# Kernel tuning notes

Measured on AMD Instinct MI355X. Metric: run time of the kernel, lower is better.

The kernel has to match this reference:

```python
import jax, jax.numpy as jnp
import numpy as np

EPS = 1e-5  # BatchNorm eps (eval mode, running_mean=0, running_var=1)

def bn(z, gamma, beta):
    s = gamma / jnp.sqrt(1.0 + EPS)
    return z * s[None, :, None, None] + beta[None, :, None, None]

def conv1d(x, w, b, pad):
    # x: (N,C,L), w: (O,C,K)
    y = jax.lax.conv_general_dilated(x, w, (1,), [(pad, pad)],
                                     dimension_numbers=('NCH', 'OIH', 'NCH'))
    return y + b[None, :, None]

def setup_inputs():
    key = jax.random.key(0)
    N, C, T, V = 128, 64, 128, 25
    S, H = 3, 8
    ig = C // 4   # gcn q/k embedding channels
    ih = C // H   # per-head channels
    ks = iter(jax.random.split(key, 40))
    rn = lambda shape, s=0.05: jax.random.normal(next(ks), shape, jnp.float32) * s
    inp = {}
    inp['x'] = jax.random.normal(next(ks), (N, C, T, V), jnp.float32)
    inp['A'] = jnp.stack([jnp.eye(V, dtype=jnp.float32)] * S) + jax.random.uniform(next(ks), (S, V, V), jnp.float32) * 0.05
    inp['alpha'] = jnp.float32(0.1)
    inp['Wq'] = rn((S, ig, C)); inp['bq'] = rn((S, ig))
    inp['Wk'] = rn((S, ig, C)); inp['bk'] = rn((S, ig))
    inp['Wf'] = rn((S, C, C)); inp['bf'] = rn((S, C))
    inp['g_gamma'] = jnp.ones((C,), jnp.float32); inp['g_beta'] = jnp.zeros((C,), jnp.float32)
    inp['W_sa'] = rn((1, C, V)); inp['b_sa'] = rn((1,))
    inp['W_ta'] = rn((1, C, 9)); inp['b_ta'] = rn((1,))
    inp['W_fc1'] = rn((C // 2, C)); inp['b_fc1'] = rn((C // 2,))
    inp['W_fc2'] = rn((C, C // 2)); inp['b_fc2'] = rn((C,))
    inp['pos_emb'] = rn((1, T, C * V), 0.02)
    inp['Wq_h'] = rn((H, ih, C)); inp['bq_h'] = rn((H, ih))
    inp['Wk_h'] = rn((H, ih, C)); inp['bk_h'] = rn((H, ih))
    inp['Wv_h'] = rn((H, ih, C)); inp['bv_h'] = rn((H, ih))
    inp['W_ffn'] = rn((C, C)); inp['b_ffn'] = rn((C,))
    inp['m_gamma'] = jnp.ones((C,), jnp.float32); inp['m_beta'] = jnp.zeros((C,), jnp.float32)
    return inp

def reference(x, A, alpha, Wq, bq, Wk, bk, Wf, bf, g_gamma, g_beta,
              W_sa, b_sa, W_ta, b_ta, W_fc1, b_fc1, W_fc2, b_fc2,
              pos_emb, Wq_h, bq_h, Wk_h, bk_h, Wv_h, bv_h,
              W_ffn, b_ffn, m_gamma, m_beta):
    N, C, T, V = x.shape
    S, ig = Wq.shape[0], Wq.shape[1]
    # ---------- unit_gcn_qkv (adaptive graph conv) ----------
    q = jnp.einsum('sic,nctv->nsitv', Wq, x) + bq[None, :, :, None, None]
    k = jnp.einsum('sic,nctv->nsitv', Wk, x) + bk[None, :, :, None, None]
    qf = q.transpose(0, 1, 4, 2, 3).reshape(N, S, V, ig * T)   # (N,S,V,ig*T)
    kf = k.reshape(N, S, ig * T, V)                            # (N,S,ig*T,V)
    att = jnp.einsum('nsvd,nsdw->nsvw', qf, kf) / jnp.float32(ig * T)
    att = jax.nn.softmax(att, axis=-2)                         # Softmax(dim=-2)
    Aad = A[None] + att * alpha                                # (N,S,V,V)
    xf = x.reshape(N, C * T, V)
    agg = jnp.einsum('ndv,nsvw->nsdw', xf, Aad).reshape(N, S, C, T, V)
    y = jnp.einsum('soc,nsctv->notv', Wf, agg) + bf.sum(0)[None, :, None, None]
    y = bn(y, g_gamma, g_beta) + x                             # down = identity (in==out)
    y = jax.nn.relu(y)
    # spatial / temporal / channel attention gates (MS-AAGCN style)
    se = y.mean(axis=2)                                        # (N,C,V)
    sa = jax.nn.sigmoid(conv1d(se, W_sa, b_sa, (V - 1) // 2))  # (N,1,V)
    y = y * sa[:, :, None, :] + y
    se = y.mean(axis=3)                                        # (N,C,T)
    ta = jax.nn.sigmoid(conv1d(se, W_ta, b_ta, 4))             # (N,1,T)
    y = y * ta[:, :, :, None] + y
    se = y.mean(axis=(2, 3))                                   # (N,C)
    ca = jax.nn.sigmoid(jax.nn.relu(se @ W_fc1.T + b_fc1) @ W_fc2.T + b_fc2)
    y = y * ca[:, :, None, None] + y
    # ---------- Multi-Head causal Temporal Attention ----------
    pe = pos_emb.reshape(1, T, C, V).transpose(0, 2, 1, 3)     # 'n t (d v)' -> 'n d t v'
    xa = y + pe
    H, ih = Wq_h.shape[0], Wq_h.shape[1]
    d = ih * V
    qh = (jnp.einsum('hoc,nctv->nhtov', Wq_h, xa) + bq_h[None, :, None, :, None]).reshape(N, H, T, d)
    kh = (jnp.einsum('hoc,nctv->nhtov', Wk_h, xa) + bk_h[None, :, None, :, None]).reshape(N, H, T, d)
    vh = (jnp.einsum('hoc,nctv->nhtov', Wv_h, xa) + bv_h[None, :, None, :, None]).reshape(N, H, T, d)
    scores = jnp.einsum('nhtd,nhsd->nhts', qh, kh) / jnp.sqrt(jnp.float32(d))
    causal = jnp.tril(jnp.ones((T, T), bool))
    scores = jnp.where(causal[None, None], scores, jnp.float32(-1e9))
    p = jax.nn.softmax(scores, axis=-1)
    oh = jnp.einsum('nhts,nhsd->nhtd', p, vh)
    # concat heads along emb dim, reinterpret '(d v)' -> channels-major layout
    z = oh.reshape(N, H, T, ih, V).transpose(0, 1, 3, 2, 4).reshape(N, C, T, V)
    z = bn(z, m_gamma, m_beta) + xa
    z = jax.nn.relu(jnp.einsum('oc,nctv->notv', W_ffn, z) + b_ffn[None, :, None, None]) + xa
    z = bn(z, m_gamma, m_beta)
    # ---------- unit residual ----------
    return jax.nn.relu(z + x)
```

## Files before the change

### kernel.cpp

```cpp
#include <hip/hip_runtime.h>
#include <hip/hip_bf16.h>

#define N_ 128
#define C_ 64
#define T_ 128
#define V_ 25
#define S_ 3
#define IG 16
#define IH 8
#define H_ 8
#define D_ 200
#define CV 1600
#define TV 3200
#define EPSB 1e-5f
#define NCHUNK 16

typedef __attribute__((ext_vector_type(8))) short short8v;
typedef __attribute__((ext_vector_type(4))) float f32x4;
#define MFMA16 __builtin_amdgcn_mfma_f32_16x16x32_bf16
#define ZIDX(r,c) ((r)*72 + ((c) ^ ((((r)>>3)&7)<<3)))

__device__ __forceinline__ float sigm(float x){ return 1.f/(1.f+expf(-x)); }
__device__ __forceinline__ float b2f(__hip_bfloat16 b){ return __bfloat162float(b); }
__device__ __forceinline__ __hip_bfloat16 f2b(float f){ return __float2bfloat16(f); }
__device__ __forceinline__ float ubl(unsigned int u){ return __uint_as_float(u<<16); }
__device__ __forceinline__ float ubh(unsigned int u){ return __uint_as_float(u & 0xffff0000u); }
__device__ __forceinline__ float sh2f(short s){ return __uint_as_float(((unsigned int)(unsigned short)s)<<16); }
__device__ __forceinline__ unsigned short f2bu(float f){
  unsigned int u = __float_as_uint(f);
  u += 0x7fff + ((u>>16)&1);
  return (unsigned short)(u>>16);
}
__device__ __forceinline__ unsigned long long pk4bf(f32x4 v){
  unsigned long long a = f2bu(v[0]);
  unsigned long long b = f2bu(v[1]);
  unsigned long long c = f2bu(v[2]);
  unsigned long long d = f2bu(v[3]);
  return a | (b<<16) | (c<<32) | (d<<48);
}

__global__ __launch_bounds__(256) void k_prep(
    const float* __restrict__ Wq, const float* __restrict__ Wk,
    const float* __restrict__ Wf,
    const float* __restrict__ Wq_h, const float* __restrict__ Wk_h,
    const float* __restrict__ Wv_h, const float* __restrict__ W_ffn,
    short* __restrict__ wqb, short* __restrict__ wkb, short* __restrict__ Wfb,
    short* __restrict__ w3b, short* __restrict__ Wffnb)
{
  const int i = blockIdx.x*256 + threadIdx.x;
  if (i < 3072){ wqb[i]=(short)f2bu(Wq[i]); wkb[i]=(short)f2bu(Wk[i]); }
  if (i < 12288) Wfb[i]=(short)f2bu(Wf[i]);
  if (i < 4096){
    w3b[i]      =(short)f2bu(Wq_h[i]);
    w3b[4096+i] =(short)f2bu(Wk_h[i]);
    w3b[8192+i] =(short)f2bu(Wv_h[i]);
    Wffnb[i]    =(short)f2bu(W_ffn[i]);
  }
}

__global__ __launch_bounds__(256) void k_gcn_att1(
    const float* __restrict__ x,
    const short* __restrict__ wqb, const float* __restrict__ bq,
    const short* __restrict__ wkb, const float* __restrict__ bk,
    float* __restrict__ attg)
{
  const int tc = blockIdx.x, n = blockIdx.y;
  const int tid = threadIdx.x;
  const int wv = tid>>6, l = tid&63, lc = l&15, lk = l>>4;
  __shared__ __align__(16) short xtb[4*32*72];
  __shared__ __align__(16) char QB[3*32*256];
  __shared__ __align__(16) char KB[3*32*256];
  __shared__ float bql[48], bkl[48];
  short8v aqf[3][2], akf[3][2];
  #pragma unroll
  for (int s=0;s<3;++s){
    #pragma unroll
    for (int ks=0;ks<2;++ks){
      aqf[s][ks] = *(const short8v*)(wqb + (s*16+lc)*64 + ks*32 + lk*8);
      akf[s][ks] = *(const short8v*)(wkb + (s*16+lc)*64 + ks*32 + lk*8);
    }
  }
  if (tid<48){ bql[tid]=bq[tid]; bkl[tid]=bk[tid]; }
  for (int i=tid;i<4*7*72;i+=256){
    int tl=i/(7*72), r=i%(7*72);
    xtb[(tl*32+25)*72 + r] = 0;
  }
  const float* xn = x + (size_t)n*C_*TV;
  #pragma unroll
  for (int tg=0; tg<2; ++tg){
    if (tg) __syncthreads();
    {
      const int base = tc*200 + tg*100;
      float4 xb[7];
      #pragma unroll
      for (int k=0;k<7;++k){
        int i = tid + k*256;
        if (i<1600){ int c=i/25,a=i%25; xb[k] = *(const float4*)(xn + (size_t)c*TV + base + a*4); }
      }
      #pragma unroll
      for (int k=0;k<7;++k){
        int i = tid + k*256;
        if (i<1600){
          int c=i/25,a=i%25;
          float xv[4]={xb[k].x,xb[k].y,xb[k].z,xb[k].w};
          #pragma unroll
          for (int j=0;j<4;++j){
            int tv=a*4+j, tl=tv/25, v=tv-tl*25;
            xtb[(tl*32+v)*72 + c] = (short)f2bu(xv[j]);
          }
        }
      }
    }
    __syncthreads();
    const int tcol = (tg*4+wv)*32;
    const int sw = (lc&7)<<4;
    #pragma unroll
    for (int s=0;s<3;++s){
      f32x4 z={0.f,0.f,0.f,0.f};
      f32x4 aq0=z,aq1=z,ak0=z,ak1=z;
      #pragma unroll
      for (int ks=0;ks<2;++ks){
        short8v b0 = *(const short8v*)(xtb + (wv*32+lc)*72 + ks*32 + lk*8);
        short8v b1 = *(const short8v*)(xtb + (wv*32+16+lc)*72 + ks*32 + lk*8);
        aq0 = MFMA16(aqf[s][ks], b0, aq0,0,0,0);
        aq1 = MFMA16(aqf[s][ks], b1, aq1,0,0,0);
        ak0 = MFMA16(akf[s][ks], b0, ak0,0,0,0);
        ak1 = MFMA16(akf[s][ks], b1, ak1,0,0,0);
      }
      f32x4 q0,q1,k0,k1;
      #pragma unroll
      for (int r=0;r<4;++r){
        float bqv=bql[s*16+lk*4+r], bkv=bkl[s*16+lk*4+r];
        q0[r]=aq0[r]+bqv; q1[r]=aq1[r]+bqv;
        k0[r]=ak0[r]+bkv; k1[r]=ak1[r]+bkv;
      }
      char* QBs = QB + s*8192;
      char* KBs = KB + s*8192;
      *(unsigned long long*)(QBs + ((lc*256      + tcol + lk*8) ^ sw)) = pk4bf(q0);
      *(unsigned long long*)(QBs + (((16+lc)*256 + tcol + lk*8) ^ sw)) = pk4bf(q1);
      *(unsigned long long*)(KBs + ((lc*256      + tcol + lk*8) ^ sw)) = pk4bf(k0);
      *(unsigned long long*)(KBs + (((16+lc)*256 + tcol + lk*8) ^ sw)) = pk4bf(k1);
    }
  }
  __syncthreads();
  const int mt = wv>>1, nt = wv&1;
  const int sw = (lc&7)<<4;
  #pragma unroll
  for (int s=0;s<3;++s){
    const char* QBs = QB + s*8192;
    const char* KBs = KB + s*8192;
    f32x4 acc = {0.f,0.f,0.f,0.f};
    #pragma unroll
    for (int ks=0;ks<4;++ks){
      short8v a = *(const short8v*)(QBs + (((mt*16+lc)*256 + ks*64 + lk*16) ^ sw));
      short8v b = *(const short8v*)(KBs + (((nt*16+lc)*256 + ks*64 + lk*16) ^ sw));
      acc = MFMA16(a,b,acc,0,0,0);
    }
    float* Ao = attg + ((size_t)tc*(N_*S_) + n*S_ + s)*(V_*V_);
    #pragma unroll
    for (int reg=0;reg<4;++reg){
      int v = mt*16 + lk*4 + reg, w = nt*16 + lc;
      if (v<V_ && w<V_) Ao[v*V_+w] = acc[reg];
    }
  }
}

__global__ __launch_bounds__(256) void k_gcn_att2(
    const float* __restrict__ attg, const float* __restrict__ A,
    const float* __restrict__ alphap, short* __restrict__ AsTg)
{
  const int ns = blockIdx.x, s = ns % S_, tid = threadIdx.x;
  __shared__ float att[V_*V_];
  short* dst = AsTg + (size_t)ns*1280;
  for (int i=tid;i<1280;i+=256) dst[i]=0;
  for (int i=tid;i<V_*V_;i+=256){
    float acc=0.f;
    #pragma unroll
    for (int tcc=0;tcc<NCHUNK;++tcc) acc += attg[((size_t)tcc*(N_*S_) + ns)*(V_*V_) + i];
    att[i]=acc;
  }
  __syncthreads();
  if (tid<V_){
    const int w=tid; const float inv=1.f/(IG*T_);
    float mx=-1e30f;
    for (int v=0;v<V_;++v) mx=fmaxf(mx, att[v*V_+w]*inv);
    float sum=0.f;
    for (int v=0;v<V_;++v){ float e=expf(att[v*V_+w]*inv-mx); att[v*V_+w]=e; sum+=e; }
    float rs=1.f/sum;
    for (int v=0;v<V_;++v) att[v*V_+w]*=rs;
  }
  __syncthreads();
  const float alpha=alphap[0];
  for (int i=tid;i<V_*V_;i+=256){
    int v=i/25, w=i%25;
    dst[w*40+v] = (short)f2bu(A[s*625+i] + alpha*att[i]);
  }
}

__global__ __launch_bounds__(256) void k_gcn_y(
    const float* __restrict__ x, const short* __restrict__ AsTg,
    const short* __restrict__ Wfb, const float* __restrict__ bfp,
    const float* __restrict__ g_gamma, const float* __restrict__ g_beta,
    __hip_bfloat16* __restrict__ y1)
{
  const int tc=blockIdx.x, n=blockIdx.y, tid=threadIdx.x;
  const int wv=tid>>6, l=tid&63, lc=l&15, lk=l>>4;
  __shared__ __align__(16) short xtb[64*136];
  __shared__ __align__(16) short AsT[3*32*40];
  __shared__ __align__(16) short aggT[112*200];
  const float* xn = x + (size_t)n*C_*TV;
  const int tv0 = tc*100;
  float4 xbuf[7];
  #pragma unroll
  for (int k=0;k<7;++k){
    int i = tid + k*256;
    if (i < 1600){
      int c=i/25, a=i%25;
      xbuf[k] = *(const float4*)(xn + (size_t)c*TV + tv0 + a*4);
    }
  }
  #pragma unroll
  for (int k=0;k<7;++k){
    int i = tid + k*256;
    if (i < 1600){
      int c=i/25, a=i%25, tv4=a*4;
      float xv[4] = {xbuf[k].x, xbuf[k].y, xbuf[k].z, xbuf[k].w};
      #pragma unroll
      for (int j=0;j<4;++j){
        int tv=tv4+j, t=tv/25, v=tv-t*25;
        xtb[c*136 + t*32 + v] = (short)f2bu(xv[j]);
      }
    }
  }
  for (int i=tid;i<64*28;i+=256){ int c=i/28, r=i%28; xtb[c*136 + (r/7)*32 + 25 + (r%7)] = 0; }
  {
    const short* As_g = AsTg + (size_t)n*3840;
    for (int i=tid;i<480;i+=256)
      *(short8v*)(AsT + i*8) = *(const short8v*)(As_g + i*8);
  }
  for (int i=tid;i<12*200;i+=256) aggT[100*200+i]=0;
  __syncthreads();
  {
    const int t = wv;
    for (int s=0;s<S_;++s){
      short8v b0 = *(const short8v*)(AsT + (s*32+lc)*40 + lk*8);
      short8v b1 = *(const short8v*)(AsT + (s*32+16+lc)*40 + lk*8);
      #pragma unroll
      for (int mt=0;mt<4;++mt){
        short8v a = *(const short8v*)(xtb + (mt*16+lc)*136 + t*32 + lk*8);
        f32x4 z={0.f,0.f,0.f,0.f};
        f32x4 acc0 = MFMA16(a,b0,z,0,0,0);
        f32x4 acc1 = MFMA16(a,b1,z,0,0,0);
        *(unsigned long long*)(aggT + (t*25+lc)*200 + s*64 + mt*16 + lk*4) = pk4bf(acc0);
        if (lc<9)
          *(unsigned long long*)(aggT + (t*25+16+lc)*200 + s*64 + mt*16 + lk*4) = pk4bf(acc1);
      }
    }
  }
  short8v af[6];
  #pragma unroll
  for (int ks=0;ks<6;++ks){
    const int s = ks>>1, c0 = (ks&1)*32 + lk*8;
    af[ks] = *(const short8v*)(Wfb + (size_t)(s*C_ + wv*16+lc)*C_ + c0);
  }
  __syncthreads();
  f32x4 acc[7];
  #pragma unroll
  for (int dt=0;dt<7;++dt) acc[dt]=(f32x4){0.f,0.f,0.f,0.f};
  #pragma unroll
  for (int dt=0;dt<7;++dt){
    #pragma unroll
    for (int ks=0;ks<6;++ks){
      short8v b = *(const short8v*)(aggT + (dt*16+lc)*200 + ks*32 + lk*8);
      acc[dt] = MFMA16(af[ks], b, acc[dt],0,0,0);
    }
  }
  const float invs = rsqrtf(1.f+EPSB);
  __hip_bfloat16* yo = y1 + (size_t)n*C_*TV;
  #pragma unroll
  for (int reg=0;reg<4;++reg){
    const int o = wv*16 + lk*4 + reg;
    const float bsum = bfp[o]+bfp[C_+o]+bfp[2*C_+o];
    const float gs = g_gamma[o]*invs, gb = g_beta[o];
    #pragma unroll
    for (int dt=0;dt<7;++dt){
      const int tv = dt*16 + lc;
      if (tv < 100){
        const int t = tv/25, v = tv - t*25;
        float xres = sh2f(xtb[o*136 + t*32 + v]);
        float val = (acc[dt][reg]+bsum)*gs + gb + xres;
        yo[(size_t)o*TV + tv0 + tv] = f2b(fmaxf(val,0.f));
      }
    }
  }
}

__global__ __launch_bounds__(256) void k_seT(const __hip_bfloat16* __restrict__ y1,
    float* __restrict__ seT)
{
  const int c=blockIdx.x, n=blockIdx.y, tid=threadIdx.x;
  const int v = tid&31, g = tid>>5;
  __shared__ float red[8][33];
  const __hip_bfloat16* yp = y1 + ((size_t)n*C_+c)*T_*V_;
  float s=0.f;
  if (v < V_){
    #pragma unroll 4
    for (int j=0;j<16;++j){
      int t = g + j*8;
      s += b2f(yp[t*V_+v]);
    }
  }
  red[g][v]=s;
  __syncthreads();
  if (tid < V_){
    float tot=0.f;
    #pragma unroll
    for (int g2=0;g2<8;++g2) tot += red[g2][tid];
    seT[((size_t)n*C_+c)*V_+tid]=tot*(1.f/T_);
  }
}

__global__ __launch_bounds__(256) void k_sa(const float* __restrict__ seT,
    const float* __restrict__ W_sa, const float* __restrict__ b_sa,
    float* __restrict__ sa)
{
  const int n=blockIdx.x, tid=threadIdx.x;
  __shared__ float sel[CV];
  __shared__ float wsl[CV];
  __shared__ float part[8][32];
  const float* se = seT + (size_t)n*C_*V_;
  for (int i=tid;i<CV;i+=256){ sel[i]=se[i]; wsl[i]=W_sa[i]; }
  __syncthreads();
  if (tid < 200){
    const int v = tid%25, cg = tid/25;
    float acc=0.f;
    for (int c=cg*8;c<cg*8+8;++c){
      #pragma unroll
      for (int k=0;k<V_;++k){
        int vv=v+k-12;
        if (vv>=0&&vv<V_) acc += sel[c*V_+vv]*wsl[c*V_+k];
      }
    }
    part[cg][v]=acc;
  }
  __syncthreads();
  if (tid<V_){
    float acc=b_sa[0];
    #pragma unroll
    for (int g=0;g<8;++g) acc+=part[g][tid];
    sa[n*V_+tid]=sigm(acc);
  }
}

__global__ __launch_bounds__(256) void k_seV(const __hip_bfloat16* __restrict__ y1,
    const float* __restrict__ sa, float* __restrict__ seV)
{
  const int c=blockIdx.x, n=blockIdx.y, tid=threadIdx.x;
  const int v = tid&31, g = tid>>5;
  __shared__ float sal[32];
  if (tid<32) sal[tid] = (tid<V_)? 1.f+sa[n*V_+tid] : 0.f;
  __syncthreads();
  const __hip_bfloat16* yp = y1 + ((size_t)n*C_+c)*T_*V_;
  float* svo = seV + ((size_t)n*C_+c)*T_;
  const float sv_ = sal[v];
  for (int j=0;j<16;++j){
    int t = g*16 + j;
    float val = (v<V_)? b2f(yp[t*V_+v])*sv_ : 0.f;
    #pragma unroll
    for (int off=16;off;off>>=1) val += __shfl_xor(val, off);
    if (v==0) svo[t]=val*(1.f/V_);
  }
}

__global__ __launch_bounds__(256) void k_ta_ca(const float* __restrict__ seV,
    const float* __restrict__ W_ta, const float* __restrict__ b_ta,
    const float* __restrict__ W_fc1, const float* __restrict__ b_fc1,
    const float* __restrict__ W_fc2, const float* __restrict__ b_fc2,
    float* __restrict__ ta, float* __restrict__ ca)
{
  const int n=blockIdx.x, tid=threadIdx.x;
  __shared__ float svl[C_*T_];
  __shared__ float wtl[C_*9];
  __shared__ float w1l[32*C_];
  __shared__ float w2l[C_*32];
  __shared__ float tal[T_];
  __shared__ float part2[2][T_];
  __shared__ float part4[C_][4];
  __shared__ float scls[C_];
  __shared__ float h1[32];
  const float* sv = seV + (size_t)n*C_*T_;
  for (int i=tid;i<C_*T_;i+=256) svl[i]=sv[i];
  for (int i=tid;i<C_*9;i+=256) wtl[i]=W_ta[i];
  for (int i=tid;i<32*C_;i+=256){ w1l[i]=W_fc1[i]; w2l[i]=W_fc2[i]; }
  __syncthreads();
  {
    const int t = tid & 127, half = tid >> 7;
    float acc = 0.f;
    for (int c=half*32; c<half*32+32; ++c){
      #pragma unroll
      for (int k=0;k<9;++k){
        int tt=t+k-4;
        if (tt>=0&&tt<T_) acc += svl[c*T_+tt]*wtl[c*9+k];
      }
    }
    part2[half][t]=acc;
  }
  __syncthreads();
  if (tid<T_){
    float s_=sigm(part2[0][tid]+part2[1][tid]+b_ta[0]);
    tal[tid]=s_; ta[n*T_+tid]=s_;
  }
  __syncthreads();
  {
    const int c = tid>>2, q = tid&3;
    float acc=0.f;
    for (int t=q*32;t<q*32+32;++t) acc += svl[c*T_+t]*(1.f+tal[t]);
    part4[c][q]=acc;
  }
  __syncthreads();
  if (tid<C_) scls[tid]=(part4[tid][0]+part4[tid][1]+part4[tid][2]+part4[tid][3])*(1.f/T_);
  __syncthreads();
  if (tid<32){
    float acc=b_fc1[tid];
    for (int c=0;c<C_;++c) acc += scls[c]*w1l[tid*C_+c];
    h1[tid]=fmaxf(acc,0.f);
  }
  __syncthreads();
  if (tid<C_){
    float acc=b_fc2[tid];
    for (int j=0;j<32;++j) acc += h1[j]*w2l[tid*32+j];
    ca[n*C_+tid]=sigm(acc);
  }
}

__global__ __launch_bounds__(256) void k_xa_qkv(
    const __hip_bfloat16* __restrict__ y1, const float* __restrict__ pos_emb,
    const float* __restrict__ sa, const float* __restrict__ ta, const float* __restrict__ ca,
    const short* __restrict__ w3b, const float* __restrict__ bq_h,
    const float* __restrict__ bk_h, const float* __restrict__ bv_h,
    __hip_bfloat16* __restrict__ xa, __hip_bfloat16* __restrict__ qb,
    __hip_bfloat16* __restrict__ kb, __hip_bfloat16* __restrict__ vb)
{
  const int tc=blockIdx.x, n=blockIdx.y, tid=threadIdx.x;
  const int wv=tid>>6, l=tid&63, lc=l&15, lk=l>>4;
  __shared__ __align__(16) short w3[192*72];
  __shared__ __align__(16) short xalT[4][32*72];
  __shared__ float bl[192];
  __shared__ float sal[32], cal[64], tgs[4];
  const int tv0 = tc*100;
  const __hip_bfloat16* y1n = y1 + (size_t)n*C_*TV;
  __hip_bfloat16* xan = xa + (size_t)n*C_*TV;
  uint2 ybuf[7];
  #pragma unroll
  for (int k=0;k<7;++k){
    int i = tid + k*256;
    if (i < 1600){
      int c=i/25, a=i%25;
      ybuf[k] = *(const uint2*)(y1n + (size_t)c*TV + tv0 + a*4);
    }
  }
  for (int i=tid;i<1536;i+=256){
    int mu=i>>3, j=i&7;
    *(short8v*)(w3 + mu*72 + j*8) = *(const short8v*)(w3b + mu*64 + j*8);
  }
  if (tid<192){
    int which=tid/C_, ho=tid%C_;
    bl[tid] = (which==0?bq_h:(which==1?bk_h:bv_h))[ho];
  }
  if (tid<32) sal[tid] = (tid<V_)? 1.f+sa[n*V_+tid] : 0.f;
  if (tid>=32 && tid<96) cal[tid-32] = 1.f+ca[n*C_+tid-32];
  if (tid>=96 && tid<100) tgs[tid-96] = 1.f+ta[n*T_+tc*4+(tid-96)];
  for (int i=tid;i<4*7*72;i+=256){
    int tl=i/(7*72), r=i%(7*72);
    xalT[tl][25*72 + r] = 0;
  }
  __syncthreads();
  #pragma unroll
  for (int k=0;k<7;++k){
    int i = tid + k*256;
    if (i < 1600){
      int c=i/25, a=i%25, tv4=a*4;
      unsigned int u0=ybuf[k].x, u1=ybuf[k].y;
      float yv[4] = {ubl(u0),ubh(u0),ubl(u1),ubh(u1)};
      const float calc = cal[c];
      unsigned long long pack = 0ull;
      #pragma unroll
      for (int j=0;j<4;++j){
        int tv=tv4+j, tl=tv/25, v=tv-tl*25;
        float val = yv[j]*sal[v]*tgs[tl]*calc + pos_emb[(size_t)(tc*4+tl)*CV + c*V_ + v];
        unsigned short b = f2bu(val);
        pack |= (unsigned long long)b << (16*j);
        xalT[tl][v*72 + c] = (short)b;
      }
      *(unsigned long long*)(xan + (size_t)c*TV + tv0 + tv4) = pack;
    }
  }
  __syncthreads();
  const int t = tc*4 + wv;
  short8v bf_[2][2];
  #pragma unroll
  for (int ks=0;ks<2;++ks){
    bf_[ks][0] = *(const short8v*)(&xalT[wv][lc*72      + ks*32 + lk*8]);
    bf_[ks][1] = *(const short8v*)(&xalT[wv][(16+lc)*72 + ks*32 + lk*8]);
  }
  #pragma unroll
  for (int mt=0;mt<12;++mt){
    f32x4 acc0 = {0.f,0.f,0.f,0.f}, acc1 = {0.f,0.f,0.f,0.f};
    #pragma unroll
    for (int ks=0;ks<2;++ks){
      short8v a = *(const short8v*)(w3 + (mt*16+lc)*72 + ks*32 + lk*8);
      acc0 = MFMA16(a, bf_[ks][0], acc0,0,0,0);
      acc1 = MFMA16(a, bf_[ks][1], acc1,0,0,0);
    }
    #pragma unroll
    for (int reg=0;reg<4;++reg){
      const int mu = mt*16 + lk*4 + reg;
      const int which = mt>>2;
      const int ho = mu & 63, h = ho>>3, o = ho&7;
      __hip_bfloat16* dst = (which==0?qb:(which==1?kb:vb))
                            + (((size_t)n*H_+h)*T_+t)*D_ + o*V_;
      const float bb = bl[mu];
      dst[lc] = f2b(acc0[reg]+bb);
      if (lc < 9) dst[16+lc] = f2b(acc1[reg]+bb);
    }
  }
}

__global__ __launch_bounds__(256) void k_attn(
    const __hip_bfloat16* __restrict__ qb, const __hip_bfloat16* __restrict__ kb,
    const __hip_bfloat16* __restrict__ vb, __hip_bfloat16* __restrict__ oh)
{
  const int bx = blockIdx.x;
  const int hh = blockIdx.y;
  const int n  = blockIdx.z;
  const int nh = n*H_ + hh;
  const int tid = threadIdx.x;
  const int wv = tid>>6, l = tid&63;
  const int lc = l&15, lg = l>>4;
  __shared__ __align__(16) char KlB[32*512];
  __shared__ __align__(16) short VT[208*40];
  __shared__ __align__(16) short Pl[64*40];
  const __hip_bfloat16* qg_ = qb + (size_t)nh*T_*D_;
  const __hip_bfloat16* kg_ = kb + (size_t)nh*T_*D_;
  const __hip_bfloat16* vg_ = vb + (size_t)nh*T_*D_;
  __hip_bfloat16* ohn = oh + (size_t)n*C_*TV;
  const float scale = 0.0707106781f;

  for (int i=tid;i<32*12;i+=256){
    int key=i/12, j=i%12;
    *(unsigned int*)(KlB + ((key*512 + 400 + j*4) ^ ((key&7)<<4))) = 0u;
  }
  for (int i=tid;i<8*40;i+=256) VT[200*40 + i] = 0;

  const int qrow = bx*64 + wv*16 + lc;
  short8v qf[7];
  {
    const short8v* qs8 = (const short8v*)(qg_ + (size_t)qrow*D_);
    #pragma unroll
    for (int ks=0;ks<7;++ks) qf[ks] = qs8[ks*4 + lg];
  }
  f32x4 oacc[13];
  #pragma unroll
  for (int i=0;i<13;++i) oacc[i] = (f32x4){0.f,0.f,0.f,0.f};
  float m[4], lsm[4];
  #pragma unroll
  for (int r=0;r<4;++r){ m[r]=-1e30f; lsm[r]=0.f; }

  const int ntiles = (bx==0)? 2 : 4;
  for (int kt=0; kt<ntiles; ++kt){
    const int j0 = kt*32;
    __syncthreads();
    {
      const short8v* ks8 = (const short8v*)(kg_ + (size_t)j0*D_);
      for (int i=tid;i<32*25;i+=256){
        int row=i/25, w=i%25;
        *(short8v*)(KlB + ((row*512 + w*16) ^ ((row&7)<<4))) = ks8[i];
      }
      const short8v* vs8 = (const short8v*)(vg_ + (size_t)j0*D_);
      for (int i=tid;i<32*25;i+=256){
        int row=i&31, w4=i>>5;
        short8v u = vs8[row*25 + w4];
        #pragma unroll
        for (int j=0;j<8;++j) VT[(w4*8+j)*40 + row] = u[j];
      }
    }
    __syncthreads();
    const bool active = (j0 <= bx*64 + wv*16 + 15);
    if (active){
      f32x4 s0 = {0.f,0.f,0.f,0.f}, s1 = {0.f,0.f,0.f,0.f};
      #pragma unroll
      for (int ks=0;ks<7;++ks){
        short8v b0 = *(const short8v*)(KlB + ((lc*512      + ks*64 + lg*16) ^ ((lc&7)<<4)));
        short8v b1 = *(const short8v*)(KlB + (((16+lc)*512 + ks*64 + lg*16) ^ ((lc&7)<<4)));
        s0 = MFMA16(qf[ks], b0, s0,0,0,0);
        s1 = MFMA16(qf[ks], b1, s1,0,0,0);
      }
      float fr[4];
      #pragma unroll
      for (int r=0;r<4;++r){
        const int qg = bx*64 + wv*16 + lg*4 + r;
        float v0 = (j0+lc    <= qg) ? s0[r]*scale : -1e30f;
        float v1 = (j0+16+lc <= qg) ? s1[r]*scale : -1e30f;
        float mx = fmaxf(v0,v1);
        #pragma unroll
        for (int off=1;off<16;off<<=1) mx = fmaxf(mx, __shfl_xor(mx, off));
        float mn = fmaxf(m[r], mx);
        fr[r] = __expf(m[r]-mn);
        float p0 = __expf(v0-mn), p1 = __expf(v1-mn);
        float ts = p0+p1;
        #pragma unroll
        for (int off=1;off<16;off<<=1) ts += __shfl_xor(ts, off);
        lsm[r] = lsm[r]*fr[r] + ts;
        m[r] = mn;
        Pl[(wv*16 + lg*4 + r)*40 + lc]      = (short)f2bu(p0);
        Pl[(wv*16 + lg*4 + r)*40 + 16 + lc] = (short)f2bu(p1);
      }
      #pragma unroll
      for (int dt=0;dt<13;++dt){
        #pragma unroll
        for (int r=0;r<4;++r) oacc[dt][r] *= fr[r];
      }
      short8v pa = *(const short8v*)(Pl + (wv*16+lc)*40 + lg*8);
      #pragma unroll
      for (int dt=0;dt<13;++dt){
        short8v b = *(const short8v*)(VT + (dt*16+lc)*40 + lg*8);
        oacc[dt] = MFMA16(pa, b, oacc[dt],0,0,0);
      }
    }
  }
  float rl[4];
  #pragma unroll
  for (int r=0;r<4;++r) rl[r] = 1.f/lsm[r];
  #pragma unroll
  for (int dt=0;dt<13;++dt){
    const int d = dt*16 + lc;
    if (d < D_){
      const int oi = d/25, v = d - oi*25;
      const int c = hh*IH + oi;
      #pragma unroll
      for (int r=0;r<4;++r){
        const int q = bx*64 + wv*16 + lg*4 + r;
        ohn[(size_t)c*TV + q*V_ + v] = f2b(oacc[dt][r]*rl[r]);
      }
    }
  }
}

__global__ __launch_bounds__(256) void k_out(
    const __hip_bfloat16* __restrict__ oh, const __hip_bfloat16* __restrict__ xa,
    const float* __restrict__ x, const short* __restrict__ Wffnb,
    const float* __restrict__ b_ffn, const float* __restrict__ m_gamma,
    const float* __restrict__ m_beta, float* __restrict__ out)
{
  const int tc = blockIdx.x, n = blockIdx.y, tid = threadIdx.x;
  const int wv = tid>>6, l = tid&63, lc = l&15, lg = l>>4;
  __shared__ __align__(16) short zT[208*72];
  __shared__ float bn_s[64], bn_b[64], bff[64];
  const float invs = rsqrtf(1.f+EPSB);
  if (tid<64){ bn_s[tid]=m_gamma[tid]*invs; bn_b[tid]=m_beta[tid]; bff[tid]=b_ffn[tid]; }
  for (int i=tid;i<8*72;i+=256) zT[200*72+i]=0;
  const int tv0 = tc*200;
  const __hip_bfloat16* xan = xa + (size_t)n*C_*TV;
  const __hip_bfloat16* ohn = oh + (size_t)n*C_*TV;
  uint4 xbuf[7], obuf[7];
  #pragma unroll
  for (int k=0;k<7;++k){
    int i = tid + k*256;
    if (i < 1600){
      int c=i/25, a=i%25;
      xbuf[k] = *(const uint4*)(xan + (size_t)c*TV + tv0 + a*8);
      obuf[k] = *(const uint4*)(ohn + (size_t)c*TV + tv0 + a*8);
    }
  }
  __syncthreads();
  #pragma unroll
  for (int k=0;k<7;++k){
    int i = tid + k*256;
    if (i < 1600){
      int c=i/25, a=i%25, tv8=a*8;
      const float s_=bn_s[c], b_=bn_b[c];
      const unsigned int* xu = (const unsigned int*)&xbuf[k];
      const unsigned int* ou = (const unsigned int*)&obuf[k];
      #pragma unroll
      for (int j=0;j<4;++j){
        zT[ZIDX(tv8+2*j,   c)] = (short)f2bu(s_*ubl(ou[j]) + b_ + ubl(xu[j]));
        zT[ZIDX(tv8+2*j+1, c)] = (short)f2bu(s_*ubh(ou[j]) + b_ + ubh(xu[j]));
      }
    }
  }
  __syncthreads();
  short8v af0 = *(const short8v*)(Wffnb + (wv*16+lc)*64 + lg*8);
  short8v af1 = *(const short8v*)(Wffnb + (wv*16+lc)*64 + 32 + lg*8);
  f32x4 acc[13];
  #pragma unroll
  for (int dt=0;dt<13;++dt) acc[dt] = (f32x4){0.f,0.f,0.f,0.f};
  #pragma unroll
  for (int dt=0;dt<13;++dt){
    short8v b0 = *(const short8v*)(zT + ZIDX(dt*16+lc, lg*8));
    short8v b1 = *(const short8v*)(zT + ZIDX(dt*16+lc, 32+lg*8));
    acc[dt] = MFMA16(af0, b0, acc[dt],0,0,0);
    acc[dt] = MFMA16(af1, b1, acc[dt],0,0,0);
  }
  __syncthreads();
  #pragma unroll
  for (int dt=0;dt<13;++dt){
    const int tv = dt*16 + lc;
    if (tv < 200){
      #pragma unroll
      for (int reg=0;reg<4;++reg){
        const int o = wv*16 + lg*4 + reg;
        zT[ZIDX(tv, o)] = (short)f2bu(acc[dt][reg]);
      }
    }
  }
  __syncthreads();
  const float* xn = x + (size_t)n*C_*TV;
  float* outn = out + (size_t)n*C_*TV;
  for (int ii=tid; ii<3200; ii+=256){
    const int c = ii/50, a = ii%50, tv4 = a*4;
    uint2 xu = *(const uint2*)(xan + (size_t)c*TV + tv0 + tv4);
    float4 xf4 = *(const float4*)(xn + (size_t)c*TV + tv0 + tv4);
    float xa4[4] = {ubl(xu.x),ubh(xu.x),ubl(xu.y),ubh(xu.y)};
    float xf[4] = {xf4.x,xf4.y,xf4.z,xf4.w};
    const float s_=bn_s[c], b_=bn_b[c], bf_=bff[c];
    float4 o4;
    float res[4];
    #pragma unroll
    for (int j=0;j<4;++j){
      float f = sh2f(zT[ZIDX(tv4+j, c)]);
      float z2 = fmaxf(f + bf_, 0.f) + xa4[j];
      float z3 = s_*z2 + b_;
      res[j] = fmaxf(z3 + xf[j], 0.f);
    }
    o4.x=res[0]; o4.y=res[1]; o4.z=res[2]; o4.w=res[3];
    *(float4*)(outn + (size_t)c*TV + tv0 + tv4) = o4;
  }
}

extern "C" void kernel_launch(void* const* d_in, const int* in_sizes, int n_in,
                              void* d_out, int out_size, void* d_ws, size_t ws_size,
                              hipStream_t stream) {
  const float* x      = (const float*)d_in[0];
  const float* A      = (const float*)d_in[1];
  const float* alphap = (const float*)d_in[2];
  const float* Wq     = (const float*)d_in[3];
  const float* bq     = (const float*)d_in[4];
  const float* Wk     = (const float*)d_in[5];
  const float* bk     = (const float*)d_in[6];
  const float* Wf     = (const float*)d_in[7];
  const float* bfp    = (const float*)d_in[8];
  const float* g_gamma= (const float*)d_in[9];
  const float* g_beta = (const float*)d_in[10];
  const float* W_sa   = (const float*)d_in[11];
  const float* b_sa   = (const float*)d_in[12];
  const float* W_ta   = (const float*)d_in[13];
  const float* b_ta   = (const float*)d_in[14];
  const float* W_fc1  = (const float*)d_in[15];
  const float* b_fc1  = (const float*)d_in[16];
  const float* W_fc2  = (const float*)d_in[17];
  const float* b_fc2  = (const float*)d_in[18];
  const float* pos_emb= (const float*)d_in[19];
  const float* Wq_h   = (const float*)d_in[20];
  const float* bq_h   = (const float*)d_in[21];
  const float* Wk_h   = (const float*)d_in[22];
  const float* bk_h   = (const float*)d_in[23];
  const float* Wv_h   = (const float*)d_in[24];
  const float* bv_h   = (const float*)d_in[25];
  const float* W_ffn  = (const float*)d_in[26];
  const float* b_ffn  = (const float*)d_in[27];
  const float* m_gamma= (const float*)d_in[28];
  const float* m_beta = (const float*)d_in[29];
  float* out = (float*)d_out;

  float* ws   = (float*)d_ws;
  float* seT  = ws;
  float* seV  = seT + 204800;
  float* sa   = seV + 1048576;
  float* ta   = sa  + 3200;
  float* ca   = ta  + 16384;
  short* wsh  = (short*)(ca + 8192);
  short* AsTg = wsh;
  short* wqb  = AsTg + 491520;
  short* wkb  = wqb + 3072;
  short* Wfb  = wkb + 3072;
  short* w3b  = Wfb + 12288;
  short* Wffnb= w3b + 12288;
  __hip_bfloat16* y1 = (__hip_bfloat16*)(Wffnb + 4096);
  __hip_bfloat16* xa = y1 + (size_t)26214400;
  __hip_bfloat16* qb = xa + (size_t)26214400;
  __hip_bfloat16* kb = qb + (size_t)26214400;
  __hip_bfloat16* vb = kb + (size_t)26214400;
  __hip_bfloat16* oh = y1;
  float* attg = (float*)y1;

  k_prep<<<48, 256, 0, stream>>>(Wq, Wk, Wf, Wq_h, Wk_h, Wv_h, W_ffn,
                                 wqb, wkb, Wfb, w3b, Wffnb);
  k_gcn_att1<<<dim3(16, N_), 256, 0, stream>>>(x, wqb, bq, wkb, bk, attg);
  k_gcn_att2<<<N_*S_, 256, 0, stream>>>(attg, A, alphap, AsTg);
  k_gcn_y<<<dim3(T_/4, N_), 256, 0, stream>>>(x, AsTg, Wfb, bfp, g_gamma, g_beta, y1);
  k_seT<<<dim3(C_, N_), 256, 0, stream>>>(y1, seT);
  k_sa<<<N_, 256, 0, stream>>>(seT, W_sa, b_sa, sa);
  k_seV<<<dim3(C_, N_), 256, 0, stream>>>(y1, sa, seV);
  k_ta_ca<<<N_, 256, 0, stream>>>(seV, W_ta, b_ta, W_fc1, b_fc1, W_fc2, b_fc2, ta, ca);
  k_xa_qkv<<<dim3(T_/4, N_), 256, 0, stream>>>(y1, pos_emb, sa, ta, ca,
      w3b, bq_h, bk_h, bv_h, xa, qb, kb, vb);
  k_attn<<<dim3(2, H_, N_), 256, 0, stream>>>(qb, kb, vb, oh);
  k_out<<<dim3(T_/8, N_), 256, 0, stream>>>(oh, xa, x, Wffnb, b_ffn, m_gamma, m_beta, out);
}
```

Before: 447.8 us.

## Prefetch next K/V tile into registers and widen FFN epilogue vectors

In the causal attention kernel, each thread now loads the next 32-row K and V tile from global memory into registers while the current tile is being computed. It then writes those registers to LDS at the top of the next iteration, with one barrier per tile moved to the end of the loop, so global latency overlaps the MFMA work. The FFN/residual epilogue now handles 8 elements per thread instead of 4 and takes the xa values from an `xbuf` register array rather than reloading them from global. The cost is extra registers for the prefetch buffers, which could reduce occupancy. The epilogue depends on `xbuf` being populated earlier in code not shown here.

```diff
diff --git a/kernel.cpp b/kernel.cpp
--- a/kernel.cpp
+++ b/kernel.cpp
@@ -567,24 +567,46 @@
   for (int r=0;r<4;++r){ m[r]=-1e30f; lsm[r]=0.f; }
 
   const int ntiles = (bx==0)? 2 : 4;
+  short8v kreg[4], vreg[4];
+  {
+    const short8v* ks8 = (const short8v*)(kg_);
+    const short8v* vs8 = (const short8v*)(vg_);
+    #pragma unroll
+    for (int k=0;k<4;++k){
+      int i = tid + k*256;
+      if (i<800){
+        kreg[k] = ks8[i];
+        vreg[k] = vs8[(i&31)*25 + (i>>5)];
+      }
+    }
+  }
   for (int kt=0; kt<ntiles; ++kt){
     const int j0 = kt*32;
+    #pragma unroll
+    for (int k=0;k<4;++k){
+      int i = tid + k*256;
+      if (i<800){
+        int row=i/25, w=i%25;
+        *(short8v*)(KlB + ((row*512 + w*16) ^ ((row&7)<<4))) = kreg[k];
+        int rowv=i&31, w4=i>>5;
+        short8v u = vreg[k];
+        #pragma unroll
+        for (int j=0;j<8;++j) VT[(w4*8+j)*40 + rowv] = u[j];
+      }
+    }
     __syncthreads();
-    {
-      const short8v* ks8 = (const short8v*)(kg_ + (size_t)j0*D_);
-      for (int i=tid;i<32*25;i+=256){
-        int row=i/25, w=i%25;
-        *(short8v*)(KlB + ((row*512 + w*16) ^ ((row&7)<<4))) = ks8[i];
-      }
-      const short8v* vs8 = (const short8v*)(vg_ + (size_t)j0*D_);
-      for (int i=tid;i<32*25;i+=256){
-        int row=i&31, w4=i>>5;
-        short8v u = vs8[row*25 + w4];
-        #pragma unroll
-        for (int j=0;j<8;++j) VT[(w4*8+j)*40 + row] = u[j];
-      }
-    }
-    __syncthreads();
+    if (kt+1 < ntiles){
+      const short8v* ks8 = (const short8v*)(kg_ + (size_t)(kt+1)*32*D_);
+      const short8v* vs8 = (const short8v*)(vg_ + (size_t)(kt+1)*32*D_);
+      #pragma unroll
+      for (int k=0;k<4;++k){
+        int i = tid + k*256;
+        if (i<800){
+          kreg[k] = ks8[i];
+          vreg[k] = vs8[(i&31)*25 + (i>>5)];
+        }
+      }
+    }
     const bool active = (j0 <= bx*64 + wv*16 + 15);
     if (active){
       f32x4 s0 = {0.f,0.f,0.f,0.f}, s1 = {0.f,0.f,0.f,0.f};
@@ -627,6 +649,7 @@
         oacc[dt] = MFMA16(pa, b, oacc[dt],0,0,0);
       }
     }
+    __syncthreads();
   }
   float rl[4];
   #pragma unroll
@@ -716,24 +739,30 @@
   __syncthreads();
   const float* xn = x + (size_t)n*C_*TV;
   float* outn = out + (size_t)n*C_*TV;
-  for (int ii=tid; ii<3200; ii+=256){
-    const int c = ii/50, a = ii%50, tv4 = a*4;
-    uint2 xu = *(const uint2*)(xan + (size_t)c*TV + tv0 + tv4);
-    float4 xf4 = *(const float4*)(xn + (size_t)c*TV + tv0 + tv4);
-    float xa4[4] = {ubl(xu.x),ubh(xu.x),ubl(xu.y),ubh(xu.y)};
-    float xf[4] = {xf4.x,xf4.y,xf4.z,xf4.w};
-    const float s_=bn_s[c], b_=bn_b[c], bf_=bff[c];
-    float4 o4;
-    float res[4];
-    #pragma unroll
-    for (int j=0;j<4;++j){
-      float f = sh2f(zT[ZIDX(tv4+j, c)]);
-      float z2 = fmaxf(f + bf_, 0.f) + xa4[j];
-      float z3 = s_*z2 + b_;
-      res[j] = fmaxf(z3 + xf[j], 0.f);
-    }
-    o4.x=res[0]; o4.y=res[1]; o4.z=res[2]; o4.w=res[3];
-    *(float4*)(outn + (size_t)c*TV + tv0 + tv4) = o4;
+  #pragma unroll
+  for (int k=0;k<7;++k){
+    int i = tid + k*256;
+    if (i < 1600){
+      const int c=i/25, a=i%25, tv8=a*8;
+      const unsigned int* xu = (const unsigned int*)&xbuf[k];
+      const float s_=bn_s[c], b_=bn_b[c], bf_=bff[c];
+      float4 xf0 = *(const float4*)(xn + (size_t)c*TV + tv0 + tv8);
+      float4 xf1 = *(const float4*)(xn + (size_t)c*TV + tv0 + tv8 + 4);
+      float xf[8] = {xf0.x,xf0.y,xf0.z,xf0.w,xf1.x,xf1.y,xf1.z,xf1.w};
+      float res[8];
+      #pragma unroll
+      for (int j=0;j<4;++j){
+        float xal = ubl(xu[j]), xah = ubh(xu[j]);
+        float f0 = sh2f(zT[ZIDX(tv8+2*j,   c)]);
+        float f1 = sh2f(zT[ZIDX(tv8+2*j+1, c)]);
+        res[2*j]   = fmaxf(s_*(fmaxf(f0+bf_,0.f)+xal)+b_ + xf[2*j],   0.f);
+        res[2*j+1] = fmaxf(s_*(fmaxf(f1+bf_,0.f)+xah)+b_ + xf[2*j+1], 0.f);
+      }
+      float4 o0 = {res[0],res[1],res[2],res[3]};
+      float4 o1 = {res[4],res[5],res[6],res[7]};
+      *(float4*)(outn + (size_t)c*TV + tv0 + tv8)     = o0;
+      *(float4*)(outn + (size_t)c*TV + tv0 + tv8 + 4) = o1;
+    }
   }
 }
 
```

Result: faster. 431.7 us, median of 2 (-3.6%).
